# Performance work log

Hardware: AMD Instinct MI355X
Metric: run time of the kernel (lower is better)

The kernel has to match this reference:

```python
import jax, jax.numpy as jnp
import numpy as np
from jax import lax

PROP_TIME = 18
K_F = 3
NUM = K_F * K_F - 1   # 8 non-center taps
IDX_REF = NUM // 2    # 4


def _bilinear(img, ys, xs):
    """img: (H,W). ys/xs: (T,H,W) absolute coords. Zero padding outside."""
    H, W = img.shape
    y0 = jnp.floor(ys)
    x0 = jnp.floor(xs)
    wy = ys - y0
    wx = xs - x0
    y0i = y0.astype(jnp.int32)
    x0i = x0.astype(jnp.int32)

    def g(yi, xi):
        valid = (yi >= 0) & (yi < H) & (xi >= 0) & (xi < W)
        v = img[jnp.clip(yi, 0, H - 1), jnp.clip(xi, 0, W - 1)]
        return jnp.where(valid, v, 0.0)

    v00 = g(y0i, x0i)
    v01 = g(y0i, x0i + 1)
    v10 = g(y0i + 1, x0i)
    v11 = g(y0i + 1, x0i + 1)
    return (v00 * (1 - wy) * (1 - wx) + v01 * (1 - wy) * wx
            + v10 * wy * (1 - wx) + v11 * wy * wx)


_sample_b = jax.vmap(_bilinear, in_axes=(0, 0, 0))  # batched over B


def setup_inputs() -> dict:
    key = jax.random.key(0)
    k1, k2, k3, k4, k5 = jax.random.split(key, 5)
    B, H, W = 4, 480, 640
    CH_G = 8
    return {
        "feat_init": jax.random.uniform(k1, (B, 1, H, W), dtype=jnp.float32),
        "guidance": jax.random.normal(k2, (B, CH_G, H, W), dtype=jnp.float32),
        "confidence": jax.random.uniform(k3, (B, 1, H, W), dtype=jnp.float32),
        "w_oa": jax.random.normal(k4, (3 * NUM, CH_G, 3, 3), dtype=jnp.float32) * 0.1,
        "b_oa": jax.random.normal(k5, (3 * NUM,), dtype=jnp.float32) * 0.01,
        "aff_scale_const": jnp.ones((1,), jnp.float32) * (0.5 * NUM),  # gamma*num (TGASS)
    }


def reference(feat_init, guidance, confidence, w_oa, b_oa, aff_scale_const):
    B, _, H, W = guidance.shape

    # offset / affinity head: Conv2d(ch_g, 3*num, k=3, pad=1)
    oa = lax.conv_general_dilated(
        guidance, w_oa, window_strides=(1, 1), padding=((1, 1), (1, 1)),
        dimension_numbers=("NCHW", "OIHW", "NCHW")) + b_oa[None, :, None, None]
    o1, o2, aff = jnp.split(oa, 3, axis=1)  # each (B, 8, H, W): dy, dx, raw aff

    # insert zero offset for the center (reference) tap -> 9 taps
    z = jnp.zeros((B, 1, H, W), o1.dtype)
    off_y = jnp.concatenate([o1[:, :IDX_REF], z, o1[:, IDX_REF:]], axis=1)  # (B,9,H,W)
    off_x = jnp.concatenate([o2[:, :IDX_REF], z, o2[:, IDX_REF:]], axis=1)

    # TGASS affinity
    aff = jnp.tanh(aff) / (aff_scale_const + 1e-8)

    # confidence propagation: 1x1 deform conv per non-center tap with w_conf=1,
    # modulation=1 -> bilinear sample of confidence at p + offset (offset detached)
    nc = jnp.array([0, 1, 2, 3, 5, 6, 7, 8])
    base_y = jnp.arange(H, dtype=jnp.float32)[:, None]
    base_x = jnp.arange(W, dtype=jnp.float32)[None, :]
    yc = base_y[None, None] + lax.stop_gradient(off_y[:, nc])  # (B,8,H,W)
    xc = base_x[None, None] + lax.stop_gradient(off_x[:, nc])
    conf_aff = _sample_b(confidence[:, 0], yc, xc)             # (B,8,H,W)
    aff = aff * conf_aff

    # absolute-sum normalization (TGASS: clamp denom at 1)
    s = jnp.sum(jnp.abs(aff), axis=1, keepdims=True) + 1e-4
    s = jnp.maximum(s, 1.0)
    aff = aff / s
    aff_ref = 1.0 - jnp.sum(aff, axis=1, keepdims=True)
    aff9 = jnp.concatenate([aff[:, :IDX_REF], aff_ref, aff[:, IDX_REF:]], axis=1)
    aff9 = jax.nn.softmax(aff9, axis=1)  # (B,9,H,W)

    # propagation sampling coords: p + kernel_tap + learned offset (fixed per iter)
    kh = jnp.repeat(jnp.arange(-1, 2, dtype=jnp.float32), 3)  # (9,)
    kw = jnp.tile(jnp.arange(-1, 2, dtype=jnp.float32), 3)
    ys = base_y[None, None] + kh[None, :, None, None] + off_y  # (B,9,H,W)
    xs = base_x[None, None] + kw[None, :, None, None] + off_x

    def step(feat, _):
        samp = _sample_b(feat[:, 0], ys, xs)                  # (B,9,H,W)
        new = jnp.sum(aff9 * samp, axis=1, keepdims=True)     # (B,1,H,W)
        return new, None

    feat_result, _ = lax.scan(step, feat_init, None, length=PROP_TIME)
    return feat_result
```

## Files before the change

### kernel.cpp

```cpp
#include <hip/hip_runtime.h>
#include <hip/hip_fp16.h>
#include <math.h>

#define BB 4
#define HH 480
#define WW 640
#define HW (HH * WW)
#define PP (BB * HW)

#define PXT 5
#define NBLK (PP / (256 * PXT))

__device__ __forceinline__ float ldz(const float* __restrict__ img, int y, int x) {
    bool v = ((unsigned)y < (unsigned)HH) & ((unsigned)x < (unsigned)WW);
    int off = v ? (y * WW + x) : 0;
    float val = img[off];
    return v ? val : 0.0f;
}

__device__ __forceinline__ void axis_map(int y0, float wy, int H,
                                         int& c0, float& t, float& s) {
    if (y0 >= 0 && y0 <= H - 2)      { c0 = y0;    t = wy;   s = 1.0f; }
    else if (y0 == -1)               { c0 = 0;     t = 0.0f; s = wy; }
    else if (y0 == H - 1)            { c0 = H - 2; t = 1.0f; s = 1.0f - wy; }
    else                             { c0 = 0;     t = 0.0f; s = 0.0f; }
}

__device__ __forceinline__ float tanh_fast(float x) {
    return 1.0f - 2.0f / (__expf(2.0f * x) + 1.0f);
}

__global__ void transpose_w_kernel(const float* __restrict__ w_oa, float* __restrict__ wT) {
    for (int i = threadIdx.x; i < 1728; i += 256) {
        const int k = i / 192;
        const int r = i - k * 192;
        const int ci = r / 24;
        const int c = r - ci * 24;
        wT[i] = w_oa[c * 72 + ci * 9 + k];
    }
}

__global__ __launch_bounds__(256) void precompute_kernel(
    const float* __restrict__ guidance,
    const float* __restrict__ confidence,
    const float* __restrict__ wT,
    const float* __restrict__ b_oa,
    const float* __restrict__ aff_scale,
    uint4* __restrict__ PK4,
    float* __restrict__ affC)
{
    const int p = blockIdx.x * 256 + threadIdx.x;
    const int b = p / HW;
    const int rem = p - b * HW;
    const int y = rem / WW;
    const int x = rem - y * WW;

    float acc[24];
    #pragma unroll
    for (int c = 0; c < 24; ++c) acc[c] = b_oa[c];

    const float* gb = guidance + (size_t)b * 8 * HW;

    #pragma unroll 1
    for (int kidx = 0; kidx < 9; ++kidx) {
        const int yy = y + kidx / 3 - 1;
        const int xx = x + kidx % 3 - 1;
        const bool valid = ((unsigned)yy < (unsigned)HH) & ((unsigned)xx < (unsigned)WW);
        const int base = valid ? (yy * WW + xx) : 0;
        float g[8];
        #pragma unroll
        for (int ci = 0; ci < 8; ++ci) {
            float v = gb[ci * HW + base];
            g[ci] = valid ? v : 0.0f;
        }
        const float* wk = wT + kidx * 192;
        #pragma unroll
        for (int ci = 0; ci < 8; ++ci) {
            const float gv = g[ci];
            #pragma unroll
            for (int c = 0; c < 24; ++c)
                acc[c] = fmaf(gv, wk[ci * 24 + c], acc[c]);
        }
    }

    const float inv_scale = 1.0f / (aff_scale[0] + 1e-8f);
    const float* cb = confidence + (size_t)b * HW;
    const float fy = (float)y, fx = (float)x;

    float affv[8];
    #pragma unroll
    for (int j = 0; j < 8; ++j) {
        const float oy = acc[j], ox = acc[8 + j];
        const float a = tanh_fast(acc[16 + j]) * inv_scale;
        const float ysj = fy + oy, xsj = fx + ox;
        const float y0f = floorf(ysj), x0f = floorf(xsj);
        const float wy = ysj - y0f, wx = xsj - x0f;
        const int y0 = (int)y0f, x0 = (int)x0f;
        const float v00 = ldz(cb, y0, x0),     v01 = ldz(cb, y0, x0 + 1);
        const float v10 = ldz(cb, y0 + 1, x0), v11 = ldz(cb, y0 + 1, x0 + 1);
        const float conf = v00 * (1.0f - wy) * (1.0f - wx) + v01 * (1.0f - wy) * wx
                         + v10 * wy * (1.0f - wx)          + v11 * wy * wx;
        affv[j] = a * conf;
    }

    float s = 1e-4f;
    #pragma unroll
    for (int j = 0; j < 8; ++j) s += fabsf(affv[j]);
    s = fmaxf(s, 1.0f);
    const float inv_s = 1.0f / s;
    float sum = 0.0f;
    #pragma unroll
    for (int j = 0; j < 8; ++j) { affv[j] *= inv_s; sum += affv[j]; }
    const float aref = 1.0f - sum;

    float m = aref;
    #pragma unroll
    for (int j = 0; j < 8; ++j) m = fmaxf(m, affv[j]);
    float e[8];
    float denom = 0.0f;
    #pragma unroll
    for (int j = 0; j < 8; ++j) { e[j] = __expf(affv[j] - m); denom += e[j]; }
    const float ec = __expf(aref - m);
    denom += ec;
    const float invden = 1.0f / denom;

    affC[p] = ec * invden * 8192.0f;

    unsigned ba[8], tt[8];
    #pragma unroll
    for (int j = 0; j < 8; ++j) {
        const int t9 = (j < 4) ? j : j + 1;
        const float khv = (float)(t9 / 3 - 1);
        const float kwv = (float)(t9 % 3 - 1);
        const float ys = (fy + khv) + acc[j];
        const float xs = (fx + kwv) + acc[8 + j];
        const float y0f = floorf(ys), x0f = floorf(xs);
        const float wy = ys - y0f, wx = xs - x0f;
        int y0c, x0c; float ty, tx, sy, sx;
        axis_map((int)y0f, wy, HH, y0c, ty, sy);
        axis_map((int)x0f, wx, WW, x0c, tx, sx);

        const float aeff = (e[j] * invden) * sy * sx;
        unsigned aq = __float2uint_rn(aeff * 8192.0f);
        aq = aq > 8191u ? 8191u : aq;
        ba[j] = ((unsigned)(y0c * WW + x0c) << 13) | aq;
        __half2 h2 = __floats2half2_rn(ty, tx);
        tt[j] = __builtin_bit_cast(unsigned, h2);
    }
    PK4[4 * p + 0] = make_uint4(ba[0], tt[0], ba[1], tt[1]);
    PK4[4 * p + 1] = make_uint4(ba[2], tt[2], ba[3], tt[3]);
    PK4[4 * p + 2] = make_uint4(ba[4], tt[4], ba[5], tt[5]);
    PK4[4 * p + 3] = make_uint4(ba[6], tt[6], ba[7], tt[7]);
}

__global__ __launch_bounds__(256) void prop_kernel(
    const float* __restrict__ src,
    float* __restrict__ dst,
    const uint4* __restrict__ PK4,
    const float* __restrict__ affC)
{
    const int tid = threadIdx.x;
    const int p0 = blockIdx.x * (256 * PXT) + tid;
    const float* fb = src + (p0 / HW) * HW;

    #pragma unroll
    for (int k = 0; k < PXT; ++k) {
        const int p = p0 + k * 256;
        const uint4 q0 = PK4[4 * p + 0];
        const uint4 q1 = PK4[4 * p + 1];
        const uint4 q2 = PK4[4 * p + 2];
        const uint4 q3 = PK4[4 * p + 3];

        float acc = affC[p] * src[p];

        auto tap = [&](unsigned bav, unsigned tw) {
            const float af = (float)(bav & 8191u);
            const float* g = fb + (bav >> 13);
            const float2 t2 = *reinterpret_cast<const float2*>(g);
            const float2 b2 = *reinterpret_cast<const float2*>(g + WW);
            const float2 t = __half22float2(__builtin_bit_cast(__half2, tw));
            const float top = fmaf(t.y, t2.y - t2.x, t2.x);
            const float bot = fmaf(t.y, b2.y - b2.x, b2.x);
            acc = fmaf(af, fmaf(t.x, bot - top, top), acc);
        };
        tap(q0.x, q0.y); tap(q0.z, q0.w);
        tap(q1.x, q1.y); tap(q1.z, q1.w);
        tap(q2.x, q2.y); tap(q2.z, q2.w);
        tap(q3.x, q3.y); tap(q3.z, q3.w);

        dst[p] = acc * (1.0f / 8192.0f);
    }
}

extern "C" void kernel_launch(void* const* d_in, const int* in_sizes, int n_in,
                              void* d_out, int out_size, void* d_ws, size_t ws_size,
                              hipStream_t stream) {
    const float* feat_init  = (const float*)d_in[0];
    const float* guidance   = (const float*)d_in[1];
    const float* confidence = (const float*)d_in[2];
    const float* w_oa       = (const float*)d_in[3];
    const float* b_oa       = (const float*)d_in[4];
    const float* aff_scale  = (const float*)d_in[5];
    float* out = (float*)d_out;
    float* ws  = (float*)d_ws;

    const size_t need = (size_t)18 * PP * sizeof(float);
    if (ws_size < need) return;

    uint4* PK4  = reinterpret_cast<uint4*>(ws);
    float* affC = ws + (size_t)16 * PP;
    float* bufA = ws + (size_t)17 * PP;
    float* wT   = bufA;

    transpose_w_kernel<<<1, 256, 0, stream>>>(w_oa, wT);
    precompute_kernel<<<PP / 256, 256, 0, stream>>>(guidance, confidence, wT, b_oa,
                                                    aff_scale, PK4, affC);

    const float* srcp = feat_init;
    for (int i = 0; i < 18; ++i) {
        float* dstp = (i & 1) ? out : bufA;
        prop_kernel<<<NBLK, 256, 0, stream>>>(srcp, dstp, PK4, affC);
        srcp = dstp;
    }
}
```

Measured before the change: 615.8 us.

## Split packed tap data into planar arrays, register-tile conv, swizzle blocks

The packed per-pixel tap records move from an interleaved 64-byte layout into four separate 16-byte planes, so each prop load is fully coalesced across the wavefront, and those loads are now nontemporal. Precompute has each thread handle four adjacent pixels, reusing the guidance row loads and weight reads across the 3x3 conv. Both kernels remap block IDs in strides of 8, presumably to spread blocks across XCDs, and prop drops to one pixel per thread with more blocks. The costs are higher register pressure in precompute and possibly lower cache locality from the block remapping.

```diff
diff --git a/kernel.cpp b/kernel.cpp
--- a/kernel.cpp
+++ b/kernel.cpp
@@ -8,15 +8,10 @@
 #define HW (HH * WW)
 #define PP (BB * HW)
 
-#define PXT 5
-#define NBLK (PP / (256 * PXT))
-
-__device__ __forceinline__ float ldz(const float* __restrict__ img, int y, int x) {
-    bool v = ((unsigned)y < (unsigned)HH) & ((unsigned)x < (unsigned)WW);
-    int off = v ? (y * WW + x) : 0;
-    float val = img[off];
-    return v ? val : 0.0f;
-}
+#define PROP_NBLK (PP / 256)
+#define PRE_NBLK  (PP / 1024)
+
+typedef unsigned u32x4 __attribute__((ext_vector_type(4)));
 
 __device__ __forceinline__ void axis_map(int y0, float wy, int H,
                                          int& c0, float& t, float& s) {
@@ -28,6 +23,13 @@
 
 __device__ __forceinline__ float tanh_fast(float x) {
     return 1.0f - 2.0f / (__expf(2.0f * x) + 1.0f);
+}
+
+__device__ __forceinline__ float ldz2(const float* __restrict__ img, int rowoff,
+                                      int xx, bool v) {
+    const int xc = v ? xx : 0;
+    const float val = img[rowoff + xc];
+    return v ? val : 0.0f;
 }
 
 __global__ void transpose_w_kernel(const float* __restrict__ w_oa, float* __restrict__ wT) {
@@ -46,150 +48,194 @@
     const float* __restrict__ wT,
     const float* __restrict__ b_oa,
     const float* __restrict__ aff_scale,
-    uint4* __restrict__ PK4,
+    u32x4* __restrict__ PKa, u32x4* __restrict__ PKb,
+    u32x4* __restrict__ PKc, u32x4* __restrict__ PKd,
     float* __restrict__ affC)
 {
-    const int p = blockIdx.x * 256 + threadIdx.x;
-    const int b = p / HW;
-    const int rem = p - b * HW;
+    const int bid = (blockIdx.x & 7) * (PRE_NBLK / 8) + (blockIdx.x >> 3);
+    const int p0 = bid * 1024 + (threadIdx.x << 2);
+    const int b = p0 / HW;
+    const int rem = p0 - b * HW;
     const int y = rem / WW;
-    const int x = rem - y * WW;
-
-    float acc[24];
-    #pragma unroll
-    for (int c = 0; c < 24; ++c) acc[c] = b_oa[c];
+    const int x0 = rem - y * WW;
 
     const float* gb = guidance + (size_t)b * 8 * HW;
 
+    float acc[4][24];
+    #pragma unroll
+    for (int q = 0; q < 4; ++q)
+        #pragma unroll
+        for (int c = 0; c < 24; ++c) acc[q][c] = b_oa[c];
+
+    bool vc[6]; int xc[6];
+    #pragma unroll
+    for (int cx = 0; cx < 6; ++cx) {
+        const int xx = x0 - 1 + cx;
+        vc[cx] = ((unsigned)xx < (unsigned)WW);
+        xc[cx] = vc[cx] ? xx : 0;
+    }
+
     #pragma unroll 1
-    for (int kidx = 0; kidx < 9; ++kidx) {
-        const int yy = y + kidx / 3 - 1;
-        const int xx = x + kidx % 3 - 1;
-        const bool valid = ((unsigned)yy < (unsigned)HH) & ((unsigned)xx < (unsigned)WW);
-        const int base = valid ? (yy * WW + xx) : 0;
-        float g[8];
-        #pragma unroll
-        for (int ci = 0; ci < 8; ++ci) {
-            float v = gb[ci * HW + base];
-            g[ci] = valid ? v : 0.0f;
-        }
-        const float* wk = wT + kidx * 192;
-        #pragma unroll
-        for (int ci = 0; ci < 8; ++ci) {
-            const float gv = g[ci];
+    for (int ky = 0; ky < 3; ++ky) {
+        const int yy = y + ky - 1;
+        const bool vrow = ((unsigned)yy < (unsigned)HH);
+        const int rowoff = vrow ? yy * WW : 0;
+
+        float g[8][6];
+        #pragma unroll
+        for (int ci = 0; ci < 8; ++ci)
             #pragma unroll
-            for (int c = 0; c < 24; ++c)
-                acc[c] = fmaf(gv, wk[ci * 24 + c], acc[c]);
+            for (int cx = 0; cx < 6; ++cx) {
+                const float v = gb[ci * HW + rowoff + xc[cx]];
+                g[ci][cx] = (vrow & vc[cx]) ? v : 0.0f;
+            }
+
+        #pragma unroll
+        for (int kx = 0; kx < 3; ++kx) {
+            const float* wk = wT + (ky * 3 + kx) * 192;
+            #pragma unroll
+            for (int ci = 0; ci < 8; ++ci) {
+                #pragma unroll
+                for (int c = 0; c < 24; ++c) {
+                    const float w = wk[ci * 24 + c];
+                    acc[0][c] = fmaf(g[ci][kx + 0], w, acc[0][c]);
+                    acc[1][c] = fmaf(g[ci][kx + 1], w, acc[1][c]);
+                    acc[2][c] = fmaf(g[ci][kx + 2], w, acc[2][c]);
+                    acc[3][c] = fmaf(g[ci][kx + 3], w, acc[3][c]);
+                }
+            }
         }
     }
 
     const float inv_scale = 1.0f / (aff_scale[0] + 1e-8f);
     const float* cb = confidence + (size_t)b * HW;
-    const float fy = (float)y, fx = (float)x;
-
-    float affv[8];
-    #pragma unroll
-    for (int j = 0; j < 8; ++j) {
-        const float oy = acc[j], ox = acc[8 + j];
-        const float a = tanh_fast(acc[16 + j]) * inv_scale;
-        const float ysj = fy + oy, xsj = fx + ox;
-        const float y0f = floorf(ysj), x0f = floorf(xsj);
-        const float wy = ysj - y0f, wx = xsj - x0f;
-        const int y0 = (int)y0f, x0 = (int)x0f;
-        const float v00 = ldz(cb, y0, x0),     v01 = ldz(cb, y0, x0 + 1);
-        const float v10 = ldz(cb, y0 + 1, x0), v11 = ldz(cb, y0 + 1, x0 + 1);
-        const float conf = v00 * (1.0f - wy) * (1.0f - wx) + v01 * (1.0f - wy) * wx
-                         + v10 * wy * (1.0f - wx)          + v11 * wy * wx;
-        affv[j] = a * conf;
-    }
-
-    float s = 1e-4f;
-    #pragma unroll
-    for (int j = 0; j < 8; ++j) s += fabsf(affv[j]);
-    s = fmaxf(s, 1.0f);
-    const float inv_s = 1.0f / s;
-    float sum = 0.0f;
-    #pragma unroll
-    for (int j = 0; j < 8; ++j) { affv[j] *= inv_s; sum += affv[j]; }
-    const float aref = 1.0f - sum;
-
-    float m = aref;
-    #pragma unroll
-    for (int j = 0; j < 8; ++j) m = fmaxf(m, affv[j]);
-    float e[8];
-    float denom = 0.0f;
-    #pragma unroll
-    for (int j = 0; j < 8; ++j) { e[j] = __expf(affv[j] - m); denom += e[j]; }
-    const float ec = __expf(aref - m);
-    denom += ec;
-    const float invden = 1.0f / denom;
-
-    affC[p] = ec * invden * 8192.0f;
-
-    unsigned ba[8], tt[8];
-    #pragma unroll
-    for (int j = 0; j < 8; ++j) {
-        const int t9 = (j < 4) ? j : j + 1;
-        const float khv = (float)(t9 / 3 - 1);
-        const float kwv = (float)(t9 % 3 - 1);
-        const float ys = (fy + khv) + acc[j];
-        const float xs = (fx + kwv) + acc[8 + j];
-        const float y0f = floorf(ys), x0f = floorf(xs);
-        const float wy = ys - y0f, wx = xs - x0f;
-        int y0c, x0c; float ty, tx, sy, sx;
-        axis_map((int)y0f, wy, HH, y0c, ty, sy);
-        axis_map((int)x0f, wx, WW, x0c, tx, sx);
-
-        const float aeff = (e[j] * invden) * sy * sx;
-        unsigned aq = __float2uint_rn(aeff * 8192.0f);
-        aq = aq > 8191u ? 8191u : aq;
-        ba[j] = ((unsigned)(y0c * WW + x0c) << 13) | aq;
-        __half2 h2 = __floats2half2_rn(ty, tx);
-        tt[j] = __builtin_bit_cast(unsigned, h2);
-    }
-    PK4[4 * p + 0] = make_uint4(ba[0], tt[0], ba[1], tt[1]);
-    PK4[4 * p + 1] = make_uint4(ba[2], tt[2], ba[3], tt[3]);
-    PK4[4 * p + 2] = make_uint4(ba[4], tt[4], ba[5], tt[5]);
-    PK4[4 * p + 3] = make_uint4(ba[6], tt[6], ba[7], tt[7]);
+    float af4[4];
+    u32x4 oa[4], ob[4], oc[4], od[4];
+
+    #pragma unroll
+    for (int q = 0; q < 4; ++q) {
+        const int x = x0 + q;
+        const float fy = (float)y, fx = (float)x;
+
+        float affv[8];
+        #pragma unroll
+        for (int j = 0; j < 8; ++j) {
+            const float oy = acc[q][j], ox = acc[q][8 + j];
+            const float a = tanh_fast(acc[q][16 + j]) * inv_scale;
+            const float ysj = fy + oy, xsj = fx + ox;
+            const float y0f = floorf(ysj), x0f = floorf(xsj);
+            const float wy = ysj - y0f, wx = xsj - x0f;
+            const int y0 = (int)y0f, x0i = (int)x0f;
+            const bool vy0 = ((unsigned)y0 < (unsigned)HH);
+            const bool vy1 = ((unsigned)(y0 + 1) < (unsigned)HH);
+            const bool vx0 = ((unsigned)x0i < (unsigned)WW);
+            const bool vx1 = ((unsigned)(x0i + 1) < (unsigned)WW);
+            const int r0 = vy0 ? y0 * WW : 0;
+            const int r1 = vy1 ? (y0 + 1) * WW : 0;
+            const float v00 = ldz2(cb, r0, x0i, vy0 & vx0);
+            const float v01 = ldz2(cb, r0, x0i + 1, vy0 & vx1);
+            const float v10 = ldz2(cb, r1, x0i, vy1 & vx0);
+            const float v11 = ldz2(cb, r1, x0i + 1, vy1 & vx1);
+            const float conf = v00 * (1.0f - wy) * (1.0f - wx) + v01 * (1.0f - wy) * wx
+                             + v10 * wy * (1.0f - wx)          + v11 * wy * wx;
+            affv[j] = a * conf;
+        }
+
+        float s = 1e-4f;
+        #pragma unroll
+        for (int j = 0; j < 8; ++j) s += fabsf(affv[j]);
+        s = fmaxf(s, 1.0f);
+        const float inv_s = 1.0f / s;
+        float sum = 0.0f;
+        #pragma unroll
+        for (int j = 0; j < 8; ++j) { affv[j] *= inv_s; sum += affv[j]; }
+        const float aref = 1.0f - sum;
+
+        float m = aref;
+        #pragma unroll
+        for (int j = 0; j < 8; ++j) m = fmaxf(m, affv[j]);
+        float e[8];
+        float denom = 0.0f;
+        #pragma unroll
+        for (int j = 0; j < 8; ++j) { e[j] = __expf(affv[j] - m); denom += e[j]; }
+        const float ec = __expf(aref - m);
+        denom += ec;
+        const float invden = 1.0f / denom;
+
+        af4[q] = ec * invden * 8192.0f;
+
+        unsigned ba[8], tt[8];
+        #pragma unroll
+        for (int j = 0; j < 8; ++j) {
+            const int t9 = (j < 4) ? j : j + 1;
+            const float khv = (float)(t9 / 3 - 1);
+            const float kwv = (float)(t9 % 3 - 1);
+            const float ys = (fy + khv) + acc[q][j];
+            const float xs = (fx + kwv) + acc[q][8 + j];
+            const float y0f = floorf(ys), x0f = floorf(xs);
+            const float wy = ys - y0f, wx = xs - x0f;
+            int y0c, x0c; float ty, tx, sy, sx;
+            axis_map((int)y0f, wy, HH, y0c, ty, sy);
+            axis_map((int)x0f, wx, WW, x0c, tx, sx);
+
+            const float aeff = (e[j] * invden) * sy * sx;
+            unsigned aq = __float2uint_rn(aeff * 8192.0f);
+            aq = aq > 8191u ? 8191u : aq;
+            ba[j] = ((unsigned)(y0c * WW + x0c) << 13) | aq;
+            __half2 h2 = __floats2half2_rn(ty, tx);
+            tt[j] = __builtin_bit_cast(unsigned, h2);
+        }
+        oa[q] = (u32x4){ba[0], tt[0], ba[1], tt[1]};
+        ob[q] = (u32x4){ba[2], tt[2], ba[3], tt[3]};
+        oc[q] = (u32x4){ba[4], tt[4], ba[5], tt[5]};
+        od[q] = (u32x4){ba[6], tt[6], ba[7], tt[7]};
+    }
+
+    #pragma unroll
+    for (int q = 0; q < 4; ++q) {
+        PKa[p0 + q] = oa[q];
+        PKb[p0 + q] = ob[q];
+        PKc[p0 + q] = oc[q];
+        PKd[p0 + q] = od[q];
+    }
+    *reinterpret_cast<float4*>(&affC[p0]) = make_float4(af4[0], af4[1], af4[2], af4[3]);
 }
 
 __global__ __launch_bounds__(256) void prop_kernel(
     const float* __restrict__ src,
     float* __restrict__ dst,
-    const uint4* __restrict__ PK4,
+    const u32x4* __restrict__ PKa, const u32x4* __restrict__ PKb,
+    const u32x4* __restrict__ PKc, const u32x4* __restrict__ PKd,
     const float* __restrict__ affC)
 {
-    const int tid = threadIdx.x;
-    const int p0 = blockIdx.x * (256 * PXT) + tid;
-    const float* fb = src + (p0 / HW) * HW;
-
-    #pragma unroll
-    for (int k = 0; k < PXT; ++k) {
-        const int p = p0 + k * 256;
-        const uint4 q0 = PK4[4 * p + 0];
-        const uint4 q1 = PK4[4 * p + 1];
-        const uint4 q2 = PK4[4 * p + 2];
-        const uint4 q3 = PK4[4 * p + 3];
-
-        float acc = affC[p] * src[p];
-
-        auto tap = [&](unsigned bav, unsigned tw) {
-            const float af = (float)(bav & 8191u);
-            const float* g = fb + (bav >> 13);
-            const float2 t2 = *reinterpret_cast<const float2*>(g);
-            const float2 b2 = *reinterpret_cast<const float2*>(g + WW);
-            const float2 t = __half22float2(__builtin_bit_cast(__half2, tw));
-            const float top = fmaf(t.y, t2.y - t2.x, t2.x);
-            const float bot = fmaf(t.y, b2.y - b2.x, b2.x);
-            acc = fmaf(af, fmaf(t.x, bot - top, top), acc);
-        };
-        tap(q0.x, q0.y); tap(q0.z, q0.w);
-        tap(q1.x, q1.y); tap(q1.z, q1.w);
-        tap(q2.x, q2.y); tap(q2.z, q2.w);
-        tap(q3.x, q3.y); tap(q3.z, q3.w);
-
-        dst[p] = acc * (1.0f / 8192.0f);
-    }
+    const int bid = (blockIdx.x & 7) * (PROP_NBLK / 8) + (blockIdx.x >> 3);
+    const int p = bid * 256 + threadIdx.x;
+    const float* fb = src + (p / HW) * HW;
+
+    const u32x4 qa = __builtin_nontemporal_load(&PKa[p]);
+    const u32x4 qb = __builtin_nontemporal_load(&PKb[p]);
+    const u32x4 qc = __builtin_nontemporal_load(&PKc[p]);
+    const u32x4 qd = __builtin_nontemporal_load(&PKd[p]);
+    const float ac = __builtin_nontemporal_load(&affC[p]);
+
+    float acc = ac * src[p];
+
+    auto tap = [&](unsigned bav, unsigned tw) {
+        const float af = (float)(bav & 8191u);
+        const float* g = fb + (bav >> 13);
+        const float2 t2 = *reinterpret_cast<const float2*>(g);
+        const float2 b2 = *reinterpret_cast<const float2*>(g + WW);
+        const float2 t = __half22float2(__builtin_bit_cast(__half2, tw));
+        const float top = fmaf(t.y, t2.y - t2.x, t2.x);
+        const float bot = fmaf(t.y, b2.y - b2.x, b2.x);
+        acc = fmaf(af, fmaf(t.x, bot - top, top), acc);
+    };
+    tap(qa.x, qa.y); tap(qa.z, qa.w);
+    tap(qb.x, qb.y); tap(qb.z, qb.w);
+    tap(qc.x, qc.y); tap(qc.z, qc.w);
+    tap(qd.x, qd.y); tap(qd.z, qd.w);
+
+    dst[p] = acc * (1.0f / 8192.0f);
 }
 
 extern "C" void kernel_launch(void* const* d_in, const int* in_sizes, int n_in,
@@ -207,19 +253,22 @@
     const size_t need = (size_t)18 * PP * sizeof(float);
     if (ws_size < need) return;
 
-    uint4* PK4  = reinterpret_cast<uint4*>(ws);
+    u32x4* PKa  = reinterpret_cast<u32x4*>(ws);
+    u32x4* PKb  = reinterpret_cast<u32x4*>(ws + (size_t)4 * PP);
+    u32x4* PKc  = reinterpret_cast<u32x4*>(ws + (size_t)8 * PP);
+    u32x4* PKd  = reinterpret_cast<u32x4*>(ws + (size_t)12 * PP);
     float* affC = ws + (size_t)16 * PP;
     float* bufA = ws + (size_t)17 * PP;
     float* wT   = bufA;
 
     transpose_w_kernel<<<1, 256, 0, stream>>>(w_oa, wT);
-    precompute_kernel<<<PP / 256, 256, 0, stream>>>(guidance, confidence, wT, b_oa,
-                                                    aff_scale, PK4, affC);
+    precompute_kernel<<<PRE_NBLK, 256, 0, stream>>>(guidance, confidence, wT, b_oa,
+                                                    aff_scale, PKa, PKb, PKc, PKd, affC);
 
     const float* srcp = feat_init;
     for (int i = 0; i < 18; ++i) {
         float* dstp = (i & 1) ? out : bufA;
-        prop_kernel<<<NBLK, 256, 0, stream>>>(srcp, dstp, PK4, affC);
+        prop_kernel<<<PROP_NBLK, 256, 0, stream>>>(srcp, dstp, PKa, PKb, PKc, PKd, affC);
         srcp = dstp;
     }
 }
```

Measured after the change: 588.4 us. -4.5%, faster.
